# Performance work log

Hardware: AMD Instinct MI355X
Metric: run time of the kernel (lower is better)

Reference implementation:

```python
import jax, jax.numpy as jnp
import numpy as np

DMODEL, DK, DV, NHEAD = 512, 64, 64, 8
MASK_VALUE = -10000000.0


def setup_inputs() -> dict:
    key = jax.random.key(0)
    ks = jax.random.split(key, 12)
    b, slen = 8, 1024
    inputs = jax.random.normal(ks[0], (b, slen, DMODEL), dtype=jnp.float32)
    mask = (jax.random.uniform(ks[1], (b, slen, slen)) < 0.1).astype(jnp.float32)
    s = 1.0 / np.sqrt(DMODEL)
    wq = jax.random.uniform(ks[2], (DK * NHEAD, DMODEL), minval=-s, maxval=s, dtype=jnp.float32)
    bq = jnp.zeros((DK * NHEAD,), jnp.float32)
    wk = jax.random.uniform(ks[3], (DK * NHEAD, DMODEL), minval=-s, maxval=s, dtype=jnp.float32)
    bk = jnp.zeros((DK * NHEAD,), jnp.float32)
    wv = jax.random.uniform(ks[4], (DV * NHEAD, DMODEL), minval=-s, maxval=s, dtype=jnp.float32)
    bv = jnp.zeros((DV * NHEAD,), jnp.float32)
    wo = jax.random.uniform(ks[5], (DMODEL, NHEAD * DV), minval=-s, maxval=s, dtype=jnp.float32)
    bo = jnp.zeros((DMODEL,), jnp.float32)
    return {"inputs": inputs, "mask": mask, "wq": wq, "bq": bq, "wk": wk,
            "bk": bk, "wv": wv, "bv": bv, "wo": wo, "bo": bo}


def mask_logits(target, mask, mask_value=MASK_VALUE):
    return target * (1.0 - mask) + mask * mask_value


def reference(inputs, mask, wq, bq, wk, bk, wv, bv, wo, bo):
    b, slen, _ = inputs.shape
    scale = np.power(DK, 0.5).astype(np.float32)
    # projections -> [b, slen, nhead, d] -> [b, nhead, slen, d]
    q = (inputs @ wq.T + bq).reshape(b, slen, NHEAD, DK).transpose(0, 2, 1, 3)
    k = (inputs @ wk.T + bk).reshape(b, slen, NHEAD, DK).transpose(0, 2, 1, 3)
    v = (inputs @ wv.T + bv).reshape(b, slen, NHEAD, DV).transpose(0, 2, 1, 3)
    # scores [b, h, s, s]
    score = jnp.einsum("bhqd,bhkd->bhqk", q, k) / scale
    m = mask[:, None, :, :]  # broadcast over heads (original repeats mask per head)
    score = mask_logits(score, m)
    attn = jax.nn.softmax(score, axis=-1)
    attn = mask_logits(attn, m, 0.0)  # second zeroing mask pass
    # dropout is identity in eval mode
    out = jnp.einsum("bhqk,bhkd->bhqd", attn, v)  # [b, h, s, dv]
    out = out.transpose(0, 2, 1, 3).reshape(b, slen, NHEAD * DV)
    return out @ wo.T + bo
```

## Files before the change

kernel.cpp:

```cpp
#include <hip/hip_runtime.h>
#include <cstdint>
#include <cstddef>

#define NHEAD 8
#define SLEN 1024

typedef __bf16 bf16x8 __attribute__((ext_vector_type(8)));
typedef float f32x4 __attribute__((ext_vector_type(4)));

__device__ inline unsigned short f2bf(float f) {
    union { float f; unsigned int u; } v; v.f = f;
    unsigned int u = v.u;
    unsigned int rounded = u + 0x7fffu + ((u >> 16) & 1u);
    return (unsigned short)(rounded >> 16);
}

__device__ inline unsigned int pack2(float a, float b) {
    return (unsigned int)f2bf(a) | ((unsigned int)f2bf(b) << 16);
}

__device__ inline unsigned int cvtpk2(float lo, float hi) {
    unsigned int r;
    asm("v_cvt_pk_bf16_f32 %0, %1, %2" : "=v"(r) : "v"(lo), "v"(hi));
    return r;
}

__device__ inline float exp2i(float x) {
    float r;
    asm("v_exp_f32 %0, %1" : "=v"(r) : "v"(x));
    return r;
}

__device__ inline void gll16(const void* g, void* l) {
    __builtin_amdgcn_global_load_lds(
        (const __attribute__((address_space(1))) unsigned int*)g,
        (__attribute__((address_space(3))) unsigned int*)l,
        16, 0, 0);
}

__device__ inline uint4 cvt8(const float* __restrict__ p) {
    float4 a = *reinterpret_cast<const float4*>(p);
    float4 b = *reinterpret_cast<const float4*>(p + 4);
    uint4 r;
    r.x = pack2(a.x, a.y);
    r.y = pack2(a.z, a.w);
    r.z = pack2(b.x, b.y);
    r.w = pack2(b.z, b.w);
    return r;
}

__global__ __launch_bounds__(256) void prep(
    const float* __restrict__ X,
    const float* __restrict__ wq, const float* __restrict__ wk,
    const float* __restrict__ wv, const float* __restrict__ wo,
    const float* __restrict__ mask,
    unsigned short* __restrict__ Xb, unsigned short* __restrict__ Wc,
    unsigned long long* __restrict__ bits)
{
    int y = blockIdx.y;
    if (y == 5) {
        int wid = (blockIdx.x * 256 + threadIdx.x) >> 6;
        int lane = threadIdx.x & 63;
        for (int s = 0; s < 16; s++) {
            size_t seg = (size_t)wid * 16 + s;
            float mv = mask[seg * 64 + lane];
            unsigned long long bb = __ballot(mv != 0.0f);
            if (lane == 0) bits[seg] = bb;
        }
        return;
    }
    const float* src;
    unsigned short* dst;
    int n;
    if (y == 0) { src = X;  dst = Xb; n = 8192 * 512; }
    else {
        src = (y == 1) ? wq : (y == 2) ? wk : (y == 3) ? wv : wo;
        dst = Wc + (size_t)(y - 1) * 262144;
        n = 262144;
    }
    int i = (blockIdx.x * 256 + threadIdx.x) * 8;
    if (i + 8 <= n) {
        uint4 v = cvt8(src + i);
        *reinterpret_cast<uint4*>(dst + i) = v;
    }
}

__global__ __launch_bounds__(256) void qkv_gemm(
    const unsigned short* __restrict__ Xb,
    const unsigned short* __restrict__ Wc,
    const float* __restrict__ bq, const float* __restrict__ bk,
    const float* __restrict__ bv,
    unsigned short* __restrict__ Qb, unsigned short* __restrict__ Kb,
    unsigned short* __restrict__ Vtb)
{
    __shared__ unsigned short SH[32768];
    const int tid = threadIdx.x;
    const int w = tid >> 6, lane = tid & 63, l15 = lane & 15, quad = lane >> 4;
    const int wm = w & 1, wn = w >> 1;
    const int r0 = blockIdx.x * 128;
    const int ytile = blockIdx.y;
    const int c0 = ytile * 128;
    const unsigned short* Wsel = Wc + (size_t)(ytile >> 2) * 262144;
    const int cw = c0 & 511;

    f32x4 zero = {0.0f, 0.0f, 0.0f, 0.0f};
    f32x4 acc[4][4];
    for (int i = 0; i < 4; i++)
        for (int j = 0; j < 4; j++) acc[i][j] = zero;

    const int lrow = lane >> 3;
    const int lcol = (lane & 7) * 8;

    auto stage = [&](int k0, int hb) {
        const unsigned short* gA = Xb + (size_t)(r0 + w * 32 + lrow) * 512 + k0 + lcol;
        const unsigned short* gB = Wsel + (size_t)(cw + w * 32 + lrow) * 512 + k0 + lcol;
        unsigned short* lA = SH + hb * 16384 + (w * 32) * 64;
        unsigned short* lB = SH + hb * 16384 + 8192 + (w * 32) * 64;
        #pragma unroll
        for (int i = 0; i < 4; i++) {
            gll16(gA + (size_t)i * 8 * 512, lA + i * 8 * 64);
            gll16(gB + (size_t)i * 8 * 512, lB + i * 8 * 64);
        }
    };

    stage(0, 0);
    for (int kt = 0; kt < 8; kt++) {
        __syncthreads();
        if (kt < 7) stage((kt + 1) * 64, (kt + 1) & 1);
        const unsigned short* As = SH + (kt & 1) * 16384;
        const unsigned short* Bs = As + 8192;
        for (int kc = 0; kc < 64; kc += 32) {
            bf16x8 af[4], bfr[4];
            for (int mi = 0; mi < 4; mi++)
                af[mi] = *reinterpret_cast<const bf16x8*>(As + (wm * 64 + mi * 16 + l15) * 64 + kc + quad * 8);
            for (int ni = 0; ni < 4; ni++)
                bfr[ni] = *reinterpret_cast<const bf16x8*>(Bs + (wn * 64 + ni * 16 + l15) * 64 + kc + quad * 8);
            for (int mi = 0; mi < 4; mi++)
                for (int ni = 0; ni < 4; ni++)
                    acc[mi][ni] = __builtin_amdgcn_mfma_f32_16x16x32_bf16(af[mi], bfr[ni], acc[mi][ni], 0, 0, 0);
        }
    }
    __syncthreads();

    const int bb = r0 >> 10;
    const int s0 = r0 & 1023;
    unsigned short* Ep = SH;

    if (ytile < 8) {
        const bool isQ = (ytile < 4);
        const float* bias = isQ ? bq : bk;
        unsigned short* dst = isQ ? Qb : Kb;
        const float scale = isQ ? 0.18033688f : 1.0f;
        const int h0 = cw >> 6;
        for (int mi = 0; mi < 4; mi++) {
            for (int ni = 0; ni < 4; ni++) {
                int col = wn * 64 + ni * 16 + l15;
                float bsv = bias[cw + col];
                for (int r = 0; r < 4; r++) {
                    int s_local = wm * 64 + mi * 16 + quad * 4 + r;
                    Ep[s_local * 136 + col] = f2bf((acc[mi][ni][r] + bsv) * scale);
                }
            }
        }
        __syncthreads();
        for (int p = 0; p < 2; p++) {
            size_t base = (((size_t)(bb * NHEAD + h0 + p)) << 10) + s0;
            for (int i = 0; i < 4; i++) {
                int flat = i * 256 + tid;
                int row = flat >> 3;
                int ch = flat & 7;
                uint4 vv = *reinterpret_cast<const uint4*>(Ep + row * 136 + p * 64 + ch * 8);
                *reinterpret_cast<uint4*>(dst + (base + row) * 64 + ch * 8) = vv;
            }
        }
    } else {
        const int h_base = (c0 - 1024) >> 6;
        for (int p = 0; p < 2; p++) {
            __syncthreads();
            if (wn == p) {
                for (int mi = 0; mi < 4; mi++) {
                    for (int ni = 0; ni < 4; ni++) {
                        int d_local = ni * 16 + l15;
                        float bias = bv[(h_base + p) * 64 + d_local];
                        for (int r = 0; r < 4; r++) {
                            int s_local = wm * 64 + mi * 16 + quad * 4 + r;
                            Ep[d_local * 136 + s_local] = f2bf(acc[mi][ni][r] + bias);
                        }
                    }
                }
            }
            __syncthreads();
            int sidx = (tid & 15) * 8;
            int drow = tid >> 4;
            for (int dg = 0; dg < 4; dg++) {
                int d = dg * 16 + drow;
                size_t dst = ((size_t)(bb * NHEAD + h_base + p) * 64 + d) * 1024 + s0;
                uint4 vv = *reinterpret_cast<const uint4*>(Ep + d * 136 + sidx);
                *reinterpret_cast<uint4*>(Vtb + dst + sidx) = vv;
            }
        }
    }
}

__global__ __launch_bounds__(256, 4) void attn_kernel(
    const unsigned short* __restrict__ Qb,
    const unsigned short* __restrict__ Kb,
    const unsigned short* __restrict__ Vtb,
    const unsigned long long* __restrict__ Mbits,
    unsigned short* __restrict__ Ob)
{
    __shared__ unsigned short KVs[3 * 64 * 72];

    const int tid = threadIdx.x;
    const int w = tid >> 6, lane = tid & 63, l15 = lane & 15, quad = lane >> 4;
    const int flat = blockIdx.x;
    const int bh = flat & 63;
    const int qt = flat >> 6;
    const int b = bh >> 3, h = bh & 7;
    const int q = qt * 64 + w * 16 + l15;
    const unsigned short* Qg = Qb + (size_t)bh * SLEN * 64;
    const unsigned short* Kg = Kb + (size_t)bh * SLEN * 64;
    const unsigned short* Vg = Vtb + (size_t)bh * 64 * SLEN;
    const unsigned long long* mrow = Mbits + ((size_t)b * SLEN + q) * 16;
    unsigned short* Ks = KVs;
    unsigned short* Vs = KVs + 4608;
    unsigned short* Prow = KVs + 9216 + (size_t)(w * 16 + l15) * 72;

    bf16x8 bq0 = *reinterpret_cast<const bf16x8*>(Qg + (size_t)q * 64 + quad * 8);
    bf16x8 bq1 = *reinterpret_cast<const bf16x8*>(Qg + (size_t)q * 64 + 32 + quad * 8);

    f32x4 zero = {0.0f, 0.0f, 0.0f, 0.0f};
    f32x4 Oacc[4];
    for (int nd = 0; nd < 4; nd++) Oacc[nd] = zero;
    float lsum0 = 0.0f, lsum1 = 0.0f;

    const int srow = tid >> 3;
    const int sc8 = (tid & 7) * 8;

    uint4 kr0, kr1, vr0, vr1;
    {
        const unsigned short* kp = Kg + (size_t)srow * 64 + sc8;
        kr0 = *reinterpret_cast<const uint4*>(kp);
        kr1 = *reinterpret_cast<const uint4*>(kp + 32 * 64);
        const unsigned short* vp = Vg + (size_t)srow * SLEN + sc8;
        vr0 = *reinterpret_cast<const uint4*>(vp);
        vr1 = *reinterpret_cast<const uint4*>(vp + (size_t)32 * SLEN);
    }

    for (int kt = 0; kt < 16; kt++) {
        *reinterpret_cast<uint4*>(Ks + srow * 72 + sc8) = kr0;
        *reinterpret_cast<uint4*>(Ks + (srow + 32) * 72 + sc8) = kr1;
        *reinterpret_cast<uint4*>(Vs + srow * 72 + sc8) = vr0;
        *reinterpret_cast<uint4*>(Vs + (srow + 32) * 72 + sc8) = vr1;
        __syncthreads();

        if (kt < 15) {
            int k0n = (kt + 1) * 64;
            const unsigned short* kp = Kg + (size_t)(k0n + srow) * 64 + sc8;
            kr0 = *reinterpret_cast<const uint4*>(kp);
            kr1 = *reinterpret_cast<const uint4*>(kp + 32 * 64);
            const unsigned short* vp = Vg + (size_t)srow * SLEN + k0n + sc8;
            vr0 = *reinterpret_cast<const uint4*>(vp);
            vr1 = *reinterpret_cast<const uint4*>(vp + (size_t)32 * SLEN);
        }

        f32x4 st[4];
        for (int ni = 0; ni < 4; ni++) {
            const unsigned short* kp = Ks + (ni * 16 + l15) * 72 + quad * 8;
            bf16x8 ka0 = *reinterpret_cast<const bf16x8*>(kp);
            bf16x8 ka1 = *reinterpret_cast<const bf16x8*>(kp + 32);
            f32x4 z = zero;
            z = __builtin_amdgcn_mfma_f32_16x16x32_bf16(ka0, bq0, z, 0, 0, 0);
            z = __builtin_amdgcn_mfma_f32_16x16x32_bf16(ka1, bq1, z, 0, 0, 0);
            st[ni] = z;
        }

        unsigned long long mv = mrow[kt] >> (quad * 4);
        unsigned int lo = (unsigned int)mv, hi = (unsigned int)(mv >> 32);
        for (int ni = 0; ni < 4; ni++) {
            unsigned int word = (ni & 2) ? hi : lo;
            int sh = (ni & 1) ? 16 : 0;
            float p0 = ((word >> (sh + 0)) & 1u) ? 0.0f : exp2i(st[ni][0]);
            float p1 = ((word >> (sh + 1)) & 1u) ? 0.0f : exp2i(st[ni][1]);
            float p2 = ((word >> (sh + 2)) & 1u) ? 0.0f : exp2i(st[ni][2]);
            float p3 = ((word >> (sh + 3)) & 1u) ? 0.0f : exp2i(st[ni][3]);
            lsum0 += (p0 + p1);
            lsum1 += (p2 + p3);
            uint2 pk;
            pk.x = cvtpk2(p0, p1);
            pk.y = cvtpk2(p2, p3);
            *reinterpret_cast<uint2*>(Prow + ni * 16 + quad * 4) = pk;
        }

        bf16x8 pb0 = *reinterpret_cast<const bf16x8*>(Prow + quad * 8);
        bf16x8 pb1 = *reinterpret_cast<const bf16x8*>(Prow + 32 + quad * 8);
        for (int nd = 0; nd < 4; nd++) {
            const unsigned short* vb = Vs + (nd * 16 + l15) * 72 + quad * 8;
            bf16x8 va0 = *reinterpret_cast<const bf16x8*>(vb);
            bf16x8 va1 = *reinterpret_cast<const bf16x8*>(vb + 32);
            Oacc[nd] = __builtin_amdgcn_mfma_f32_16x16x32_bf16(va0, pb0, Oacc[nd], 0, 0, 0);
            Oacc[nd] = __builtin_amdgcn_mfma_f32_16x16x32_bf16(va1, pb1, Oacc[nd], 0, 0, 0);
        }
        __syncthreads();
    }

    float l = lsum0 + lsum1;
    l += __shfl_xor(l, 16);
    l += __shfl_xor(l, 32);
    float inv = (l > 0.0f) ? (1.0f / l) : 0.0f;
    for (int nd = 0; nd < 4; nd++) {
        uint2 o;
        o.x = cvtpk2(Oacc[nd][0] * inv, Oacc[nd][1] * inv);
        o.y = cvtpk2(Oacc[nd][2] * inv, Oacc[nd][3] * inv);
        *reinterpret_cast<uint2*>(Ob + ((size_t)(b * SLEN + q)) * 512 + h * 64 + nd * 16 + quad * 4) = o;
    }
}

__global__ __launch_bounds__(256) void out_gemm(
    const unsigned short* __restrict__ Ob,
    const unsigned short* __restrict__ Wob,
    const float* __restrict__ bo,
    float* __restrict__ out)
{
    __shared__ unsigned short As[64 * 64 + 128 * 64];
    unsigned short* Bs = As + 64 * 64;
    const int tid = threadIdx.x;
    const int w = tid >> 6, lane = tid & 63, l15 = lane & 15, quad = lane >> 4;
    const int r0 = blockIdx.x * 64;
    const int c0 = blockIdx.y * 128;

    f32x4 zero = {0.0f, 0.0f, 0.0f, 0.0f};
    f32x4 acc[4][2];
    for (int i = 0; i < 4; i++)
        for (int j = 0; j < 2; j++) acc[i][j] = zero;

    const int lrow = lane >> 3;
    const int lcol = (lane & 7) * 8;

    for (int k0 = 0; k0 < 512; k0 += 64) {
        const unsigned short* gA = Ob + (size_t)(r0 + w * 16 + lrow) * 512 + k0 + lcol;
        unsigned short* lA = As + (w * 16) * 64;
        #pragma unroll
        for (int i = 0; i < 2; i++)
            gll16(gA + (size_t)i * 8 * 512, lA + i * 8 * 64);
        const unsigned short* gB = Wob + (size_t)(c0 + w * 32 + lrow) * 512 + k0 + lcol;
        unsigned short* lB = Bs + (w * 32) * 64;
        #pragma unroll
        for (int i = 0; i < 4; i++)
            gll16(gB + (size_t)i * 8 * 512, lB + i * 8 * 64);
        __syncthreads();
        for (int kc = 0; kc < 64; kc += 32) {
            bf16x8 af[4], bfr[2];
            for (int mi = 0; mi < 4; mi++)
                af[mi] = *reinterpret_cast<const bf16x8*>(As + (mi * 16 + l15) * 64 + kc + quad * 8);
            for (int ni = 0; ni < 2; ni++)
                bfr[ni] = *reinterpret_cast<const bf16x8*>(Bs + (w * 32 + ni * 16 + l15) * 64 + kc + quad * 8);
            for (int mi = 0; mi < 4; mi++)
                for (int ni = 0; ni < 2; ni++)
                    acc[mi][ni] = __builtin_amdgcn_mfma_f32_16x16x32_bf16(af[mi], bfr[ni], acc[mi][ni], 0, 0, 0);
        }
        __syncthreads();
    }

    for (int mi = 0; mi < 4; mi++) {
        int grow_base = r0 + mi * 16 + quad * 4;
        for (int ni = 0; ni < 2; ni++) {
            int gcol = c0 + w * 32 + ni * 16 + l15;
            float bias = bo[gcol];
            for (int r = 0; r < 4; r++) {
                int grow = grow_base + r;
                out[(size_t)grow * 512 + gcol] = acc[mi][ni][r] + bias;
            }
        }
    }
}

extern "C" void kernel_launch(void* const* d_in, const int* in_sizes, int n_in,
                              void* d_out, int out_size, void* d_ws, size_t ws_size,
                              hipStream_t stream) {
    (void)in_sizes; (void)n_in; (void)out_size; (void)ws_size;
    const float* x    = (const float*)d_in[0];
    const float* mask = (const float*)d_in[1];
    const float* wq   = (const float*)d_in[2];
    const float* bq   = (const float*)d_in[3];
    const float* wk   = (const float*)d_in[4];
    const float* bk   = (const float*)d_in[5];
    const float* wv   = (const float*)d_in[6];
    const float* bv   = (const float*)d_in[7];
    const float* wo   = (const float*)d_in[8];
    const float* bo   = (const float*)d_in[9];
    float* out = (float*)d_out;

    char* ws = (char*)d_ws;
    unsigned short* Qb   = (unsigned short*)(ws);
    unsigned short* Kb   = (unsigned short*)(ws + 8388608);
    unsigned short* Vtb  = (unsigned short*)(ws + 16777216);
    unsigned short* XO   = (unsigned short*)(ws + 25165824);
    unsigned short* Wc   = (unsigned short*)(ws + 33554432);
    unsigned long long* Mbits = (unsigned long long*)(ws + 35651584);

    prep<<<dim3(2048, 6), 256, 0, stream>>>(x, wq, wk, wv, wo, mask, XO, Wc, Mbits);
    qkv_gemm<<<dim3(64, 12), 256, 0, stream>>>(XO, Wc, bq, bk, bv, Qb, Kb, Vtb);
    attn_kernel<<<dim3(1024), 256, 0, stream>>>(Qb, Kb, Vtb, Mbits, XO );
    out_gemm<<<dim3(128, 4), 256, 0, stream>>>(XO , Wc + 3 * 262144, bo, out);
}
```

Before: 181.0 us.

## Fuse X fp32-to-bf16 conversion into QKV GEMM A-tile staging

Removes the separate prep pass that converted the 8192x512 input from fp32 to bf16 and wrote it to a workspace buffer. The QKV GEMM now loads fp32 X tiles into registers one k-step ahead, converts them with packed bf16 conversion, and writes them to LDS, while the weights still use direct global-to-LDS loads. This saves the extra write and re-read of the converted input but doubles the bytes read for A per GEMM block. X is also re-read by all 12 column tiles, which adds register pressure and replaces the async loads for the A operand with synchronous ones.

```diff
diff --git a/kernel.cpp b/kernel.cpp
--- a/kernel.cpp
+++ b/kernel.cpp
@@ -50,15 +50,14 @@
 }
 
 __global__ __launch_bounds__(256) void prep(
-    const float* __restrict__ X,
     const float* __restrict__ wq, const float* __restrict__ wk,
     const float* __restrict__ wv, const float* __restrict__ wo,
     const float* __restrict__ mask,
-    unsigned short* __restrict__ Xb, unsigned short* __restrict__ Wc,
+    unsigned short* __restrict__ Wc,
     unsigned long long* __restrict__ bits)
 {
     int y = blockIdx.y;
-    if (y == 5) {
+    if (y == 4) {
         int wid = (blockIdx.x * 256 + threadIdx.x) >> 6;
         int lane = threadIdx.x & 63;
         for (int s = 0; s < 16; s++) {
@@ -69,15 +68,9 @@
         }
         return;
     }
-    const float* src;
-    unsigned short* dst;
-    int n;
-    if (y == 0) { src = X;  dst = Xb; n = 8192 * 512; }
-    else {
-        src = (y == 1) ? wq : (y == 2) ? wk : (y == 3) ? wv : wo;
-        dst = Wc + (size_t)(y - 1) * 262144;
-        n = 262144;
-    }
+    const float* src = (y == 0) ? wq : (y == 1) ? wk : (y == 2) ? wv : wo;
+    unsigned short* dst = Wc + (size_t)y * 262144;
+    const int n = 262144;
     int i = (blockIdx.x * 256 + threadIdx.x) * 8;
     if (i + 8 <= n) {
         uint4 v = cvt8(src + i);
@@ -86,7 +79,7 @@
 }
 
 __global__ __launch_bounds__(256) void qkv_gemm(
-    const unsigned short* __restrict__ Xb,
+    const float* __restrict__ X,
     const unsigned short* __restrict__ Wc,
     const float* __restrict__ bq, const float* __restrict__ bk,
     const float* __restrict__ bv,
@@ -111,22 +104,48 @@
     const int lrow = lane >> 3;
     const int lcol = (lane & 7) * 8;
 
-    auto stage = [&](int k0, int hb) {
-        const unsigned short* gA = Xb + (size_t)(r0 + w * 32 + lrow) * 512 + k0 + lcol;
+    float4 arA[4], arB[4];
+
+    auto loadA = [&](int k0) {
+        const float* gA = X + (size_t)(r0 + w * 32 + lrow) * 512 + k0 + lcol;
+        #pragma unroll
+        for (int i = 0; i < 4; i++) {
+            arA[i] = *reinterpret_cast<const float4*>(gA + (size_t)i * 8 * 512);
+            arB[i] = *reinterpret_cast<const float4*>(gA + (size_t)i * 8 * 512 + 4);
+        }
+    };
+    auto writeA = [&](int hb) {
+        unsigned short* lA = SH + hb * 16384 + (w * 32 + lrow) * 64 + lcol;
+        #pragma unroll
+        for (int i = 0; i < 4; i++) {
+            uint4 u;
+            u.x = cvtpk2(arA[i].x, arA[i].y);
+            u.y = cvtpk2(arA[i].z, arA[i].w);
+            u.z = cvtpk2(arB[i].x, arB[i].y);
+            u.w = cvtpk2(arB[i].z, arB[i].w);
+            *reinterpret_cast<uint4*>(lA + i * 8 * 64) = u;
+        }
+    };
+    auto stageB = [&](int k0, int hb) {
         const unsigned short* gB = Wsel + (size_t)(cw + w * 32 + lrow) * 512 + k0 + lcol;
-        unsigned short* lA = SH + hb * 16384 + (w * 32) * 64;
         unsigned short* lB = SH + hb * 16384 + 8192 + (w * 32) * 64;
         #pragma unroll
-        for (int i = 0; i < 4; i++) {
-            gll16(gA + (size_t)i * 8 * 512, lA + i * 8 * 64);
+        for (int i = 0; i < 4; i++)
             gll16(gB + (size_t)i * 8 * 512, lB + i * 8 * 64);
-        }
     };
 
-    stage(0, 0);
+    loadA(0);
+    writeA(0);
+    stageB(0, 0);
+    loadA(64);
+
     for (int kt = 0; kt < 8; kt++) {
         __syncthreads();
-        if (kt < 7) stage((kt + 1) * 64, (kt + 1) & 1);
+        if (kt < 7) {
+            writeA((kt + 1) & 1);
+            stageB((kt + 1) * 64, (kt + 1) & 1);
+            if (kt < 6) loadA((kt + 2) * 64);
+        }
         const unsigned short* As = SH + (kt & 1) * 16384;
         const unsigned short* Bs = As + 8192;
         for (int kc = 0; kc < 64; kc += 32) {
@@ -395,12 +414,12 @@
     unsigned short* Qb   = (unsigned short*)(ws);
     unsigned short* Kb   = (unsigned short*)(ws + 8388608);
     unsigned short* Vtb  = (unsigned short*)(ws + 16777216);
-    unsigned short* XO   = (unsigned short*)(ws + 25165824);
+    unsigned short* Obuf = (unsigned short*)(ws + 25165824);
     unsigned short* Wc   = (unsigned short*)(ws + 33554432);
     unsigned long long* Mbits = (unsigned long long*)(ws + 35651584);
 
-    prep<<<dim3(2048, 6), 256, 0, stream>>>(x, wq, wk, wv, wo, mask, XO, Wc, Mbits);
-    qkv_gemm<<<dim3(64, 12), 256, 0, stream>>>(XO, Wc, bq, bk, bv, Qb, Kb, Vtb);
-    attn_kernel<<<dim3(1024), 256, 0, stream>>>(Qb, Kb, Vtb, Mbits, XO );
-    out_gemm<<<dim3(128, 4), 256, 0, stream>>>(XO , Wc + 3 * 262144, bo, out);
-}
+    prep<<<dim3(2048, 5), 256, 0, stream>>>(wq, wk, wv, wo, mask, Wc, Mbits);
+    qkv_gemm<<<dim3(64, 12), 256, 0, stream>>>(x, Wc, bq, bk, bv, Qb, Kb, Vtb);
+    attn_kernel<<<dim3(1024), 256, 0, stream>>>(Qb, Kb, Vtb, Mbits, Obuf);
+    out_gemm<<<dim3(128, 4), 256, 0, stream>>>(Obuf, Wc + 3 * 262144, bo, out);
+}
```

Measured after the change: 190.7 us. 5.3% more time.
